# Kernel tuning notes

Measured on AMD Instinct MI355X. Metric: run time of the kernel, lower is better.

The kernel has to match this reference:

```python
import jax, jax.numpy as jnp
import numpy as np

WINDOW_SIZE = 512
CAUSAL = True

def _sliding_window_mask(seq_len, window_size, causal):
    i = jnp.arange(seq_len)[:, None]
    j = jnp.arange(seq_len)[None, :]
    mask = (j >= i - window_size + 1) & (j <= i)
    if causal:
        mask = mask & (j <= i)
    return mask  # [S, S] bool, True = attend


def setup_inputs() -> dict:
    key = jax.random.key(0)
    k1, k2, k3 = jax.random.split(key, 3)
    B, S, D = 16, 4096, 64
    q = jax.random.normal(k1, (B, S, D), dtype=jnp.float32)
    k = jax.random.normal(k2, (B, S, D), dtype=jnp.float32)
    v = jax.random.normal(k3, (B, S, D), dtype=jnp.float32)
    return {"q": q, "k": k, "v": v}


def reference(q, k, v):
    B, S, D = q.shape
    scale = D ** -0.5
    mask = _sliding_window_mask(S, WINDOW_SIZE, CAUSAL)  # [S, S]
    scores = jnp.einsum("bqd,bkd->bqk", q, k) * scale    # [B, S, S]
    mask_value = -jnp.finfo(scores.dtype).max
    scores = jnp.where(mask[None, :, :], scores, mask_value)
    attn = jax.nn.softmax(scores, axis=-1)
    out = jnp.einsum("bqk,bkd->bqd", attn, v)            # [B, S, D]
    return out
```

## Files before the change

### kernel.cpp

```cpp
#include <hip/hip_runtime.h>

#define BATCH 16
#define SEQ   4096
#define DIM   64
#define WIN   512

constexpr int BM = 64;
constexpr int BN = 64;
constexpr int KS = DIM + 8;
constexpr int VS = BN + 4;
constexpr int OS = DIM + 4;
constexpr float QSCALE  = 0.125f * 1.44269504088896340736f;
constexpr float MASKVAL = -3.0e38f;

typedef _Float16 f16x2 __attribute__((ext_vector_type(2)));
typedef _Float16 f16x4 __attribute__((ext_vector_type(4)));
typedef _Float16 f16x8 __attribute__((ext_vector_type(8)));
typedef float    f32x4 __attribute__((ext_vector_type(4)));

__device__ __forceinline__ f16x2 pk2(float a, float b) {
    return __builtin_bit_cast(f16x2, __builtin_amdgcn_cvt_pkrtz(a, b));
}

__global__ __launch_bounds__(256)
void swa_kernel(const float* __restrict__ qg, const float* __restrict__ kg,
                const float* __restrict__ vg, float* __restrict__ outg) {
    __shared__ __align__(16) char smem[(BN * KS + DIM * VS) * 2];
    _Float16* Ksh = (_Float16*)smem;
    _Float16* Vsh = (_Float16*)(smem + BN * KS * 2);
    float*    Osh = (float*)smem;

    const int tid  = threadIdx.x;
    const int lane = tid & 63;
    const int wave = tid >> 6;
    const int lr   = lane & 15;
    const int quad = lane >> 4;

    const int b     = blockIdx.y;
    const int qblk  = blockIdx.x;
    const int qrow0 = qblk * BM;
    const int wr0   = qrow0 + wave * 16;
    const int q     = wr0 + lr;

    const float* qb = qg + (size_t)b * SEQ * DIM;
    const float* kb = kg + (size_t)b * SEQ * DIM;
    const float* vb = vg + (size_t)b * SEQ * DIM;
    float*       ob = outg + (size_t)b * SEQ * DIM;

    const float* qp = qb + (size_t)q * DIM + quad * 8;
    const float4 a0 = *(const float4*)(qp + 0);
    const float4 a1 = *(const float4*)(qp + 4);
    const float4 a2 = *(const float4*)(qp + 32);
    const float4 a3 = *(const float4*)(qp + 36);
    union { f16x8 v; f16x2 h[4]; } uq0, uq1;
    uq0.h[0] = pk2(a0.x * QSCALE, a0.y * QSCALE);
    uq0.h[1] = pk2(a0.z * QSCALE, a0.w * QSCALE);
    uq0.h[2] = pk2(a1.x * QSCALE, a1.y * QSCALE);
    uq0.h[3] = pk2(a1.z * QSCALE, a1.w * QSCALE);
    uq1.h[0] = pk2(a2.x * QSCALE, a2.y * QSCALE);
    uq1.h[1] = pk2(a2.z * QSCALE, a2.w * QSCALE);
    uq1.h[2] = pk2(a3.x * QSCALE, a3.y * QSCALE);
    uq1.h[3] = pk2(a3.z * QSCALE, a3.w * QSCALE);
    const f16x8 qf0 = uq0.v, qf1 = uq1.v;

    f32x4 o[4];
    #pragma unroll
    for (int mi = 0; mi < 4; ++mi) o[mi] = (f32x4){0.f, 0.f, 0.f, 0.f};
    float m_run = -1e30f, l_run = 0.f;

    const int t0 = (qrow0 > (WIN - 1)) ? (qrow0 - (WIN - 1)) >> 6 : 0;
    const int t1 = qblk;

    for (int t = t0; t <= t1; ++t) {
        __syncthreads();
        #pragma unroll
        for (int i = 0; i < 4; ++i) {
            const int fid = tid + 256 * i;
            const int row = fid >> 4;
            const int c4  = (fid & 15) * 4;
            const size_t g = (size_t)(t * BN + row) * DIM + c4;
            const float4 kv = *(const float4*)&kb[g];
            union { f16x4 v; f16x2 h[2]; } uk;
            uk.h[0] = pk2(kv.x, kv.y);
            uk.h[1] = pk2(kv.z, kv.w);
            *(f16x4*)&Ksh[row * KS + c4] = uk.v;
            const float4 vv = *(const float4*)&vb[g];
            Vsh[(c4 + 0) * VS + row] = (_Float16)vv.x;
            Vsh[(c4 + 1) * VS + row] = (_Float16)vv.y;
            Vsh[(c4 + 2) * VS + row] = (_Float16)vv.z;
            Vsh[(c4 + 3) * VS + row] = (_Float16)vv.w;
        }
        __syncthreads();

        if (t * BN + (BN - 1) < wr0 - (WIN - 1)) continue;
        const int kbase = t * BN;

        f32x4 sc[4];
        #pragma unroll
        for (int mt = 0; mt < 4; ++mt) {
            const f16x8 kf0 = *(const f16x8*)&Ksh[(mt * 16 + lr) * KS + quad * 8];
            const f16x8 kf1 = *(const f16x8*)&Ksh[(mt * 16 + lr) * KS + 32 + quad * 8];
            f32x4 s = (f32x4){0.f, 0.f, 0.f, 0.f};
            s = __builtin_amdgcn_mfma_f32_16x16x32_f16(kf0, qf0, s, 0, 0, 0);
            s = __builtin_amdgcn_mfma_f32_16x16x32_f16(kf1, qf1, s, 0, 0, 0);
            sc[mt] = s;
        }

        const bool edge = (kbase < wr0 + 15 - (WIN - 1)) || (kbase + BN - 1 > wr0);
        if (edge) {
            #pragma unroll
            for (int mt = 0; mt < 4; ++mt) {
                #pragma unroll
                for (int r = 0; r < 4; ++r) {
                    const int key = kbase + mt * 16 + quad * 4 + r;
                    sc[mt][r] = ((unsigned)(q - key) < (unsigned)WIN) ? sc[mt][r] : MASKVAL;
                }
            }
        }

        float mt_ = MASKVAL;
        #pragma unroll
        for (int mtile = 0; mtile < 4; ++mtile)
            #pragma unroll
            for (int r = 0; r < 4; ++r) mt_ = fmaxf(mt_, sc[mtile][r]);
        mt_ = fmaxf(mt_, __shfl_xor(mt_, 16));
        mt_ = fmaxf(mt_, __shfl_xor(mt_, 32));
        const float mn    = fmaxf(m_run, mt_);
        const float alpha = exp2f(m_run - mn);
        m_run = mn;

        f16x4 pb[4];
        float ls = 0.f;
        #pragma unroll
        for (int nt = 0; nt < 4; ++nt) {
            const float p0 = exp2f(sc[nt][0] - mn);
            const float p1 = exp2f(sc[nt][1] - mn);
            const float p2 = exp2f(sc[nt][2] - mn);
            const float p3 = exp2f(sc[nt][3] - mn);
            ls += (p0 + p1) + (p2 + p3);
            union { f16x4 v; f16x2 h[2]; } up;
            up.h[0] = pk2(p0, p1);
            up.h[1] = pk2(p2, p3);
            pb[nt] = up.v;
        }
        l_run = l_run * alpha + ls;
        #pragma unroll
        for (int mi = 0; mi < 4; ++mi) o[mi] = o[mi] * alpha;

        #pragma unroll
        for (int nt = 0; nt < 4; ++nt) {
            #pragma unroll
            for (int mi = 0; mi < 4; ++mi) {
                const f16x4 vf = *(const f16x4*)&Vsh[(mi * 16 + lr) * VS + nt * 16 + quad * 4];
                o[mi] = __builtin_amdgcn_mfma_f32_16x16x16f16(vf, pb[nt], o[mi], 0, 0, 0);
            }
        }
    }

    l_run += __shfl_xor(l_run, 16);
    l_run += __shfl_xor(l_run, 32);
    const float inv = 1.0f / l_run;

    __syncthreads();
    float* Ow = Osh + wave * 16 * OS;
    #pragma unroll
    for (int mi = 0; mi < 4; ++mi) {
        float4 st;
        st.x = o[mi][0] * inv; st.y = o[mi][1] * inv;
        st.z = o[mi][2] * inv; st.w = o[mi][3] * inv;
        *(float4*)&Ow[lr * OS + mi * 16 + quad * 4] = st;
    }
    #pragma unroll
    for (int j = 0; j < 4; ++j) {
        const int qq = quad + 4 * j;
        const int d4 = lr * 4;
        const float4 vst = *(const float4*)&Ow[qq * OS + d4];
        *(float4*)&ob[(size_t)(wr0 + qq) * DIM + d4] = vst;
    }
}

extern "C" void kernel_launch(void* const* d_in, const int* in_sizes, int n_in,
                              void* d_out, int out_size, void* d_ws, size_t ws_size,
                              hipStream_t stream) {
    (void)in_sizes; (void)n_in; (void)out_size; (void)d_ws; (void)ws_size;
    const float* q = (const float*)d_in[0];
    const float* k = (const float*)d_in[1];
    const float* v = (const float*)d_in[2];
    float* out = (float*)d_out;
    dim3 grid(SEQ / BM, BATCH);
    swa_kernel<<<grid, dim3(256), 0, stream>>>(q, k, v, out);
}
```

Measured before the change: 129.2 us.

## Double query tile to 128 rows and prefetch next K/V tile into registers

Each block now covers 128 query rows with 512 threads (8 waves), so every staged K/V tile is shared by twice as many query rows. The next K/V tile's global loads are issued into registers before computing on the current tile and written to LDS after a barrier, overlapping global latency with MFMA work. Waves skip compute for tiles outside their own window, since the block now spans more tiles than any one wave needs. Shared memory is sized for the output staging buffer. The cost is higher register pressure from the prefetch registers, fewer blocks in the grid, and more idle per-wave iterations near the window edges.

New measurement: 109.9 us. 1.18x faster.

```diff
diff --git a/kernel.cpp b/kernel.cpp
--- a/kernel.cpp
+++ b/kernel.cpp
@@ -5,8 +5,9 @@
 #define DIM   64
 #define WIN   512
 
-constexpr int BM = 64;
+constexpr int BM = 128;
 constexpr int BN = 64;
+constexpr int NTHREADS = 512;
 constexpr int KS = DIM + 8;
 constexpr int VS = BN + 4;
 constexpr int OS = DIM + 4;
@@ -22,10 +23,23 @@
     return __builtin_bit_cast(f16x2, __builtin_amdgcn_cvt_pkrtz(a, b));
 }
 
-__global__ __launch_bounds__(256)
+__device__ __forceinline__ void stage_kv(_Float16* __restrict__ Ksh, _Float16* __restrict__ Vsh,
+                                         const float4& kv, const float4& vv,
+                                         int row, int c4) {
+    union { f16x4 v; f16x2 h[2]; } uk;
+    uk.h[0] = pk2(kv.x, kv.y);
+    uk.h[1] = pk2(kv.z, kv.w);
+    *(f16x4*)&Ksh[row * KS + c4] = uk.v;
+    Vsh[(c4 + 0) * VS + row] = (_Float16)vv.x;
+    Vsh[(c4 + 1) * VS + row] = (_Float16)vv.y;
+    Vsh[(c4 + 2) * VS + row] = (_Float16)vv.z;
+    Vsh[(c4 + 3) * VS + row] = (_Float16)vv.w;
+}
+
+__global__ __launch_bounds__(NTHREADS)
 void swa_kernel(const float* __restrict__ qg, const float* __restrict__ kg,
                 const float* __restrict__ vg, float* __restrict__ outg) {
-    __shared__ __align__(16) char smem[(BN * KS + DIM * VS) * 2];
+    __shared__ __align__(16) char smem[BM * OS * 4];
     _Float16* Ksh = (_Float16*)smem;
     _Float16* Vsh = (_Float16*)(smem + BN * KS * 2);
     float*    Osh = (float*)smem;
@@ -46,6 +60,9 @@
     const float* kb = kg + (size_t)b * SEQ * DIM;
     const float* vb = vg + (size_t)b * SEQ * DIM;
     float*       ob = outg + (size_t)b * SEQ * DIM;
+
+    const int row0 = tid >> 4;
+    const int c4   = (tid & 15) * 4;
 
     const float* qp = qb + (size_t)q * DIM + quad * 8;
     const float4 a0 = *(const float4*)(qp + 0);
@@ -69,99 +86,105 @@
     float m_run = -1e30f, l_run = 0.f;
 
     const int t0 = (qrow0 > (WIN - 1)) ? (qrow0 - (WIN - 1)) >> 6 : 0;
-    const int t1 = qblk;
+    const int t1 = (qrow0 + BM - 1) >> 6;
+
+    {
+        const size_t g0 = (size_t)(t0 * BN + row0) * DIM + c4;
+        stage_kv(Ksh, Vsh, *(const float4*)&kb[g0], *(const float4*)&vb[g0], row0, c4);
+        const size_t g1 = g0 + (size_t)32 * DIM;
+        stage_kv(Ksh, Vsh, *(const float4*)&kb[g1], *(const float4*)&vb[g1], row0 + 32, c4);
+    }
+    __syncthreads();
 
     for (int t = t0; t <= t1; ++t) {
-        __syncthreads();
-        #pragma unroll
-        for (int i = 0; i < 4; ++i) {
-            const int fid = tid + 256 * i;
-            const int row = fid >> 4;
-            const int c4  = (fid & 15) * 4;
-            const size_t g = (size_t)(t * BN + row) * DIM + c4;
-            const float4 kv = *(const float4*)&kb[g];
-            union { f16x4 v; f16x2 h[2]; } uk;
-            uk.h[0] = pk2(kv.x, kv.y);
-            uk.h[1] = pk2(kv.z, kv.w);
-            *(f16x4*)&Ksh[row * KS + c4] = uk.v;
-            const float4 vv = *(const float4*)&vb[g];
-            Vsh[(c4 + 0) * VS + row] = (_Float16)vv.x;
-            Vsh[(c4 + 1) * VS + row] = (_Float16)vv.y;
-            Vsh[(c4 + 2) * VS + row] = (_Float16)vv.z;
-            Vsh[(c4 + 3) * VS + row] = (_Float16)vv.w;
+        const bool have_next = (t < t1);
+        float4 kpre0, kpre1, vpre0, vpre1;
+        if (have_next) {
+            const size_t g0 = (size_t)((t + 1) * BN + row0) * DIM + c4;
+            kpre0 = *(const float4*)&kb[g0];
+            vpre0 = *(const float4*)&vb[g0];
+            const size_t g1 = g0 + (size_t)32 * DIM;
+            kpre1 = *(const float4*)&kb[g1];
+            vpre1 = *(const float4*)&vb[g1];
+        }
+
+        const int kbase = t * BN;
+        const bool active = (kbase + BN - 1 >= wr0 - (WIN - 1)) && (kbase <= wr0 + 15);
+        if (active) {
+            f32x4 sc[4];
+            #pragma unroll
+            for (int mt = 0; mt < 4; ++mt) {
+                const f16x8 kf0 = *(const f16x8*)&Ksh[(mt * 16 + lr) * KS + quad * 8];
+                const f16x8 kf1 = *(const f16x8*)&Ksh[(mt * 16 + lr) * KS + 32 + quad * 8];
+                f32x4 s = (f32x4){0.f, 0.f, 0.f, 0.f};
+                s = __builtin_amdgcn_mfma_f32_16x16x32_f16(kf0, qf0, s, 0, 0, 0);
+                s = __builtin_amdgcn_mfma_f32_16x16x32_f16(kf1, qf1, s, 0, 0, 0);
+                sc[mt] = s;
+            }
+
+            const bool edge = (kbase < wr0 + 15 - (WIN - 1)) || (kbase + BN - 1 > wr0);
+            if (edge) {
+                #pragma unroll
+                for (int mt = 0; mt < 4; ++mt) {
+                    #pragma unroll
+                    for (int r = 0; r < 4; ++r) {
+                        const int key = kbase + mt * 16 + quad * 4 + r;
+                        sc[mt][r] = ((unsigned)(q - key) < (unsigned)WIN) ? sc[mt][r] : MASKVAL;
+                    }
+                }
+            }
+
+            float mt_ = MASKVAL;
+            #pragma unroll
+            for (int mtile = 0; mtile < 4; ++mtile)
+                #pragma unroll
+                for (int r = 0; r < 4; ++r) mt_ = fmaxf(mt_, sc[mtile][r]);
+            mt_ = fmaxf(mt_, __shfl_xor(mt_, 16));
+            mt_ = fmaxf(mt_, __shfl_xor(mt_, 32));
+            const float mn    = fmaxf(m_run, mt_);
+            const float alpha = exp2f(m_run - mn);
+            m_run = mn;
+
+            f16x4 pb[4];
+            float ls = 0.f;
+            #pragma unroll
+            for (int nt = 0; nt < 4; ++nt) {
+                const float p0 = exp2f(sc[nt][0] - mn);
+                const float p1 = exp2f(sc[nt][1] - mn);
+                const float p2 = exp2f(sc[nt][2] - mn);
+                const float p3 = exp2f(sc[nt][3] - mn);
+                ls += (p0 + p1) + (p2 + p3);
+                union { f16x4 v; f16x2 h[2]; } up;
+                up.h[0] = pk2(p0, p1);
+                up.h[1] = pk2(p2, p3);
+                pb[nt] = up.v;
+            }
+            l_run = l_run * alpha + ls;
+            #pragma unroll
+            for (int mi = 0; mi < 4; ++mi) o[mi] = o[mi] * alpha;
+
+            #pragma unroll
+            for (int nt = 0; nt < 4; ++nt) {
+                #pragma unroll
+                for (int mi = 0; mi < 4; ++mi) {
+                    const f16x4 vf = *(const f16x4*)&Vsh[(mi * 16 + lr) * VS + nt * 16 + quad * 4];
+                    o[mi] = __builtin_amdgcn_mfma_f32_16x16x16f16(vf, pb[nt], o[mi], 0, 0, 0);
+                }
+            }
+        }
+
+        __builtin_amdgcn_s_barrier();
+        if (have_next) {
+            stage_kv(Ksh, Vsh, kpre0, vpre0, row0, c4);
+            stage_kv(Ksh, Vsh, kpre1, vpre1, row0 + 32, c4);
         }
         __syncthreads();
-
-        if (t * BN + (BN - 1) < wr0 - (WIN - 1)) continue;
-        const int kbase = t * BN;
-
-        f32x4 sc[4];
-        #pragma unroll
-        for (int mt = 0; mt < 4; ++mt) {
-            const f16x8 kf0 = *(const f16x8*)&Ksh[(mt * 16 + lr) * KS + quad * 8];
-            const f16x8 kf1 = *(const f16x8*)&Ksh[(mt * 16 + lr) * KS + 32 + quad * 8];
-            f32x4 s = (f32x4){0.f, 0.f, 0.f, 0.f};
-            s = __builtin_amdgcn_mfma_f32_16x16x32_f16(kf0, qf0, s, 0, 0, 0);
-            s = __builtin_amdgcn_mfma_f32_16x16x32_f16(kf1, qf1, s, 0, 0, 0);
-            sc[mt] = s;
-        }
-
-        const bool edge = (kbase < wr0 + 15 - (WIN - 1)) || (kbase + BN - 1 > wr0);
-        if (edge) {
-            #pragma unroll
-            for (int mt = 0; mt < 4; ++mt) {
-                #pragma unroll
-                for (int r = 0; r < 4; ++r) {
-                    const int key = kbase + mt * 16 + quad * 4 + r;
-                    sc[mt][r] = ((unsigned)(q - key) < (unsigned)WIN) ? sc[mt][r] : MASKVAL;
-                }
-            }
-        }
-
-        float mt_ = MASKVAL;
-        #pragma unroll
-        for (int mtile = 0; mtile < 4; ++mtile)
-            #pragma unroll
-            for (int r = 0; r < 4; ++r) mt_ = fmaxf(mt_, sc[mtile][r]);
-        mt_ = fmaxf(mt_, __shfl_xor(mt_, 16));
-        mt_ = fmaxf(mt_, __shfl_xor(mt_, 32));
-        const float mn    = fmaxf(m_run, mt_);
-        const float alpha = exp2f(m_run - mn);
-        m_run = mn;
-
-        f16x4 pb[4];
-        float ls = 0.f;
-        #pragma unroll
-        for (int nt = 0; nt < 4; ++nt) {
-            const float p0 = exp2f(sc[nt][0] - mn);
-            const float p1 = exp2f(sc[nt][1] - mn);
-            const float p2 = exp2f(sc[nt][2] - mn);
-            const float p3 = exp2f(sc[nt][3] - mn);
-            ls += (p0 + p1) + (p2 + p3);
-            union { f16x4 v; f16x2 h[2]; } up;
-            up.h[0] = pk2(p0, p1);
-            up.h[1] = pk2(p2, p3);
-            pb[nt] = up.v;
-        }
-        l_run = l_run * alpha + ls;
-        #pragma unroll
-        for (int mi = 0; mi < 4; ++mi) o[mi] = o[mi] * alpha;
-
-        #pragma unroll
-        for (int nt = 0; nt < 4; ++nt) {
-            #pragma unroll
-            for (int mi = 0; mi < 4; ++mi) {
-                const f16x4 vf = *(const f16x4*)&Vsh[(mi * 16 + lr) * VS + nt * 16 + quad * 4];
-                o[mi] = __builtin_amdgcn_mfma_f32_16x16x16f16(vf, pb[nt], o[mi], 0, 0, 0);
-            }
-        }
     }
 
     l_run += __shfl_xor(l_run, 16);
     l_run += __shfl_xor(l_run, 32);
     const float inv = 1.0f / l_run;
 
-    __syncthreads();
     float* Ow = Osh + wave * 16 * OS;
     #pragma unroll
     for (int mi = 0; mi < 4; ++mi) {
@@ -188,5 +211,5 @@
     const float* v = (const float*)d_in[2];
     float* out = (float*)d_out;
     dim3 grid(SEQ / BM, BATCH);
-    swa_kernel<<<grid, dim3(256), 0, stream>>>(q, k, v, out);
-}
+    swa_kernel<<<grid, dim3(NTHREADS), 0, stream>>>(q, k, v, out);
+}
```
